# Optimization experiments

Measured on AMD Instinct MI355X. Metric: run time of the kernel, lower is better.

## Reference

```python
import jax, jax.numpy as jnp
import numpy as np

D = 1024
H = 16
HD = D // H


def setup_inputs() -> dict:
    key = jax.random.key(0)
    ks = jax.random.split(key, 9)
    s = 1.0 / np.sqrt(D)
    x = jax.random.normal(ks[0], (2, 2048, D), dtype=jnp.float32)
    Wq = jax.random.uniform(ks[1], (D, D), jnp.float32, -s, s)
    bq = jax.random.uniform(ks[2], (D,), jnp.float32, -s, s)
    Wk = jax.random.uniform(ks[3], (D, D), jnp.float32, -s, s)
    bk = jax.random.uniform(ks[4], (D,), jnp.float32, -s, s)
    Wv = jax.random.uniform(ks[5], (D, D), jnp.float32, -s, s)
    bv = jax.random.uniform(ks[6], (D,), jnp.float32, -s, s)
    Wo = jax.random.uniform(ks[7], (D, D), jnp.float32, -s, s)
    bo = jax.random.uniform(ks[8], (D,), jnp.float32, -s, s)
    return {"x": x, "Wq": Wq, "bq": bq, "Wk": Wk, "bk": bk,
            "Wv": Wv, "bv": bv, "Wo": Wo, "bo": bo}


def reference(x, Wq, bq, Wk, bk, Wv, bv, Wo, bo):
    B, S, _ = x.shape
    # project and split heads -> [B, H, S, HD]
    def split(t):
        return t.reshape(B, S, H, HD).transpose(0, 2, 1, 3)
    q = split(x @ Wq + bq)
    k = split(x @ Wk + bk)
    v = split(x @ Wv + bv)
    scores = jnp.einsum('bhqd,bhkd->bhqk', q, k) / np.sqrt(HD).astype(np.float32)
    attn = jax.nn.softmax(scores, axis=-1)
    ctx = jnp.einsum('bhqk,bhkd->bhqd', attn, v)  # [B,H,S,HD]
    ctx = ctx.transpose(0, 2, 1, 3).reshape(B, S, D)
    return ctx @ Wo + bo
```

## Files before the change

kernel.cpp:

```cpp
#include <hip/hip_runtime.h>
#include <hip/hip_bf16.h>
#include <math.h>

#define BB 2
#define SS 2048
#define DD 1024
#define HH 16
#define HD 64
#define MM (BB * SS)

typedef __bf16 bf16;
typedef __attribute__((ext_vector_type(8))) __bf16 bf16x8;
typedef __attribute__((ext_vector_type(4))) __bf16 bf16x4;
typedef __attribute__((ext_vector_type(4))) float f32x4;

#define QSCL 0.18033688011112042f

__device__ __forceinline__ void glds16(const bf16* g, bf16* l) {
    __builtin_amdgcn_global_load_lds(
        (const __attribute__((address_space(1))) void*)g,
        (__attribute__((address_space(3))) void*)l, 16, 0, 0);
}

__device__ __forceinline__ unsigned cvtpk_bf16(float a, float b) {
    unsigned r;
    asm("v_cvt_pk_bf16_f32 %0, %1, %2" : "=v"(r) : "v"(a), "v"(b));
    return r;
}

__global__ __launch_bounds__(256) void cvt_x(const float* __restrict__ x,
                                             bf16* __restrict__ xb) {
    int i = (blockIdx.x * 256 + threadIdx.x) * 4;
    float4 v = *(const float4*)(x + i);
    bf16x4 o;
    o[0] = (bf16)v.x; o[1] = (bf16)v.y; o[2] = (bf16)v.z; o[3] = (bf16)v.w;
    *(bf16x4*)(xb + i) = o;
}

__global__ __launch_bounds__(256) void cvt_w(
    const float* __restrict__ W0, const float* __restrict__ W1,
    const float* __restrict__ W2, const float* __restrict__ W3,
    bf16* __restrict__ Wt) {
    const float* W = (blockIdx.z == 0) ? W0 : (blockIdx.z == 1) ? W1
                   : (blockIdx.z == 2) ? W2 : W3;
    bf16* dst = Wt + (size_t)blockIdx.z * DD * DD;

    __shared__ float T[64][65];
    int k0 = blockIdx.y * 64, n0 = blockIdx.x * 64;
    int tr = threadIdx.x >> 4, tc = (threadIdx.x & 15) * 4;
#pragma unroll
    for (int u = 0; u < 4; u++) {
        int r = tr + u * 16;
        float4 v = *(const float4*)&W[(size_t)(k0 + r) * DD + n0 + tc];
        T[tc + 0][r] = v.x; T[tc + 1][r] = v.y;
        T[tc + 2][r] = v.z; T[tc + 3][r] = v.w;
    }
    __syncthreads();
#pragma unroll
    for (int u = 0; u < 4; u++) {
        int r = tr + u * 16;
        bf16x4 o;
        o[0] = (bf16)T[r][tc + 0]; o[1] = (bf16)T[r][tc + 1];
        o[2] = (bf16)T[r][tc + 2]; o[3] = (bf16)T[r][tc + 3];
        *(bf16x4*)&dst[(size_t)(n0 + r) * DD + k0 + tc] = o;
    }
}

__global__ __launch_bounds__(256) void vt_kernel(const bf16* __restrict__ V,
                                                 bf16* __restrict__ Vt) {
    const int bh = blockIdx.y;
    const int b = bh >> 4, h = bh & 15;
    const int s0 = blockIdx.x * 64;

    __shared__ bf16 T[64][72];
    const int r = threadIdx.x >> 2;
    const int c0 = (threadIdx.x & 3) * 16;

    const bf16* src = V + ((size_t)(b * SS + s0 + r)) * DD + h * HD + c0;
    *(bf16x8*)&T[r][c0]     = *(const bf16x8*)(src);
    *(bf16x8*)&T[r][c0 + 8] = *(const bf16x8*)(src + 8);
    __syncthreads();

    bf16x8 o0, o1;
#pragma unroll
    for (int i = 0; i < 8; i++) o0[i] = T[c0 + i][r];
#pragma unroll
    for (int i = 0; i < 8; i++) o1[i] = T[c0 + 8 + i][r];
    bf16* dst = Vt + ((size_t)bh * HD + r) * SS + s0 + c0;
    *(bf16x8*)dst       = o0;
    *(bf16x8*)(dst + 8) = o1;
}

__global__ __launch_bounds__(256) void mfma_gemm(
    const bf16* __restrict__ A, const bf16* __restrict__ Wt0,
    const float* __restrict__ b0, const float* __restrict__ b1,
    const float* __restrict__ b2,
    bf16* __restrict__ o0, bf16* __restrict__ o1, bf16* __restrict__ o2) {
    const int z = blockIdx.z;
    const bf16* Wt = Wt0 + (size_t)z * DD * DD;
    const float* bias = (z == 0) ? b0 : (z == 1) ? b1 : b2;
    bf16* dstb = (z == 0) ? o0 : (z == 1) ? o1 : o2;
    const float scl = (z == 0) ? QSCL : 1.0f;

    __shared__ __align__(16) bf16 As[128 * 64];
    __shared__ __align__(16) bf16 Bs[128 * 64];

    const int tid = threadIdx.x;
    const int lane = tid & 63;
    const int w = tid >> 6;
    const int l15 = lane & 15, quad = lane >> 4;
    const int m0 = blockIdx.y * 128;
    const int n0 = blockIdx.x * 128;
    const int mw = (w & 1) * 64;
    const int nw = (w >> 1) * 64;

    f32x4 acc[4][4];
#pragma unroll
    for (int i = 0; i < 4; i++)
#pragma unroll
        for (int j = 0; j < 4; j++) acc[i][j] = (f32x4){0.f, 0.f, 0.f, 0.f};

    for (int kt = 0; kt < DD; kt += 64) {
        __syncthreads();
#pragma unroll
        for (int u = 0; u < 4; u++) {
            int j = tid + u * 256;
            int row = j >> 3, cp = j & 7;
            int c = cp ^ (row & 7);
            glds16(A  + (size_t)(m0 + row) * DD + kt + c * 8, &As[j * 8]);
            glds16(Wt + (size_t)(n0 + row) * DD + kt + c * 8, &Bs[j * 8]);
        }
        __syncthreads();

#pragma unroll
        for (int kh = 0; kh < 2; kh++) {
            bf16x8 af[4], bf[4];
#pragma unroll
            for (int i = 0; i < 4; i++) {
                int ra = mw + i * 16 + l15;
                int ja = ra * 8 + ((kh * 4 + quad) ^ (ra & 7));
                af[i] = *(const bf16x8*)&As[ja * 8];
                int rb = nw + i * 16 + l15;
                int jb = rb * 8 + ((kh * 4 + quad) ^ (rb & 7));
                bf[i] = *(const bf16x8*)&Bs[jb * 8];
            }
#pragma unroll
            for (int i = 0; i < 4; i++)
#pragma unroll
                for (int j = 0; j < 4; j++)
                    acc[i][j] = __builtin_amdgcn_mfma_f32_16x16x32_bf16(
                        af[i], bf[j], acc[i][j], 0, 0, 0);
        }
    }

    float bcol[4];
#pragma unroll
    for (int j = 0; j < 4; j++) bcol[j] = bias[n0 + nw + j * 16 + l15];

#pragma unroll
    for (int i = 0; i < 4; i++)
#pragma unroll
        for (int j = 0; j < 4; j++)
#pragma unroll
            for (int r = 0; r < 4; r++) {
                int row = m0 + mw + i * 16 + quad * 4 + r;
                int col = n0 + nw + j * 16 + l15;
                dstb[(size_t)row * DD + col] =
                    (bf16)((acc[i][j][r] + bcol[j]) * scl);
            }
}

__global__ __launch_bounds__(256) void mfma_gemm_out(
    const bf16* __restrict__ A, const bf16* __restrict__ Wt,
    const float* __restrict__ bias, float* __restrict__ out) {
    __shared__ __align__(16) bf16 As[64 * 64];
    __shared__ __align__(16) bf16 Bs[128 * 64];

    const int tid = threadIdx.x;
    const int lane = tid & 63;
    const int w = tid >> 6;
    const int l15 = lane & 15, quad = lane >> 4;
    const int m0 = blockIdx.y * 64;
    const int n0 = blockIdx.x * 128;
    const int mw = (w & 1) * 32;
    const int nw = (w >> 1) * 64;

    f32x4 acc[2][4];
#pragma unroll
    for (int i = 0; i < 2; i++)
#pragma unroll
        for (int j = 0; j < 4; j++) acc[i][j] = (f32x4){0.f, 0.f, 0.f, 0.f};

    for (int kt = 0; kt < DD; kt += 64) {
        __syncthreads();
#pragma unroll
        for (int u = 0; u < 2; u++) {
            int j = tid + u * 256;
            int row = j >> 3, c = (j & 7) ^ (row & 7);
            glds16(A + (size_t)(m0 + row) * DD + kt + c * 8, &As[j * 8]);
        }
#pragma unroll
        for (int u = 0; u < 4; u++) {
            int j = tid + u * 256;
            int row = j >> 3, c = (j & 7) ^ (row & 7);
            glds16(Wt + (size_t)(n0 + row) * DD + kt + c * 8, &Bs[j * 8]);
        }
        __syncthreads();

#pragma unroll
        for (int kh = 0; kh < 2; kh++) {
            bf16x8 af[2], bf[4];
#pragma unroll
            for (int i = 0; i < 2; i++) {
                int ra = mw + i * 16 + l15;
                int ja = ra * 8 + ((kh * 4 + quad) ^ (ra & 7));
                af[i] = *(const bf16x8*)&As[ja * 8];
            }
#pragma unroll
            for (int j = 0; j < 4; j++) {
                int rb = nw + j * 16 + l15;
                int jb = rb * 8 + ((kh * 4 + quad) ^ (rb & 7));
                bf[j] = *(const bf16x8*)&Bs[jb * 8];
            }
#pragma unroll
            for (int i = 0; i < 2; i++)
#pragma unroll
                for (int j = 0; j < 4; j++)
                    acc[i][j] = __builtin_amdgcn_mfma_f32_16x16x32_bf16(
                        af[i], bf[j], acc[i][j], 0, 0, 0);
        }
    }

    float bcol[4];
#pragma unroll
    for (int j = 0; j < 4; j++) bcol[j] = bias[n0 + nw + j * 16 + l15];

#pragma unroll
    for (int i = 0; i < 2; i++)
#pragma unroll
        for (int j = 0; j < 4; j++)
#pragma unroll
            for (int r = 0; r < 4; r++) {
                int row = m0 + mw + i * 16 + quad * 4 + r;
                int col = n0 + nw + j * 16 + l15;
                out[(size_t)row * DD + col] = acc[i][j][r] + bcol[j];
            }
}

__global__ __launch_bounds__(256) void mfma_attn(
    const bf16* __restrict__ Qb, const bf16* __restrict__ Kb,
    const bf16* __restrict__ Vtg, bf16* __restrict__ ctxb) {
    __shared__ __align__(16) bf16 Ks[2][64 * 64];
    __shared__ __align__(16) bf16 Vs[2][64 * 64];
    __shared__ __align__(16) bf16 Ps[4][16 * 64];

    const int tid = threadIdx.x;
    const int lane = tid & 63;
    const int w = tid >> 6;
    const int l15 = lane & 15, quad = lane >> 4;
    const int bh = blockIdx.y;
    const int b = bh >> 4, h = bh & 15;
    const int q0 = blockIdx.x * 64;
    const size_t mb = (size_t)b * SS;
    const int hc = h * HD;
    const bf16* Vt_bh = Vtg + (size_t)bh * HD * SS;
    bf16* Pw = &Ps[w][0];

    bf16x8 qf[2];
#pragma unroll
    for (int kh = 0; kh < 2; kh++)
        qf[kh] = *(const bf16x8*)&Qb[(mb + q0 + w * 16 + l15) * DD +
                                     hc + kh * 32 + quad * 8];

    bf16x8 onev;
#pragma unroll
    for (int i = 0; i < 8; i++) onev[i] = (bf16)1.0f;

    int koff[4][2], voff[4][2], prd[2], pwr[4];
#pragma unroll
    for (int kb = 0; kb < 4; kb++) {
        int rk = kb * 16 + l15;
#pragma unroll
        for (int kh = 0; kh < 2; kh++)
            koff[kb][kh] = (rk * 8 + ((kh * 4 + quad) ^ (rk & 7))) * 8;
    }
#pragma unroll
    for (int nb = 0; nb < 4; nb++) {
        int rv = nb * 16 + l15;
#pragma unroll
        for (int kh = 0; kh < 2; kh++)
            voff[nb][kh] = (rv * 8 + ((kh * 4 + quad) ^ (rv & 7))) * 8;
    }
#pragma unroll
    for (int kh = 0; kh < 2; kh++)
        prd[kh] = l15 * 64 + (((kh * 4 + quad) ^ (l15 & 7)) << 3);
#pragma unroll
    for (int kb = 0; kb < 4; kb++) {
        int cw = kb * 2 + (quad >> 1);
        pwr[kb] = l15 * 64 + ((cw ^ (l15 & 7)) << 3) + (quad & 1) * 4;
    }

    const bf16* gK[2]; const bf16* gV[2]; int lo_[2];
#pragma unroll
    for (int u = 0; u < 2; u++) {
        int j = tid + u * 256;
        int row = j >> 3, cp = j & 7;
        int c = cp ^ (row & 7);
        gK[u] = Kb + (mb + row) * DD + hc + c * 8;
        gV[u] = Vt_bh + (size_t)row * SS + c * 8;
        lo_[u] = j * 8;
    }

    f32x4 o[4], lsum;
    lsum = (f32x4){0.f, 0.f, 0.f, 0.f};
#pragma unroll
    for (int nb = 0; nb < 4; nb++) o[nb] = (f32x4){0.f, 0.f, 0.f, 0.f};

#pragma unroll
    for (int u = 0; u < 2; u++) {
        glds16(gK[u], &Ks[0][lo_[u]]);  gK[u] += 64 * DD;
        glds16(gV[u], &Vs[0][lo_[u]]);  gV[u] += 64;
    }
    __syncthreads();

    for (int it = 0; it < SS / 64; ++it) {
        const int buf = it & 1;
        if (it + 1 < SS / 64) {
#pragma unroll
            for (int u = 0; u < 2; u++) {
                glds16(gK[u], &Ks[buf ^ 1][lo_[u]]);  gK[u] += 64 * DD;
                glds16(gV[u], &Vs[buf ^ 1][lo_[u]]);  gV[u] += 64;
            }
        }

        f32x4 sc[4];
#pragma unroll
        for (int kb = 0; kb < 4; kb++) sc[kb] = (f32x4){0.f, 0.f, 0.f, 0.f};
#pragma unroll
        for (int kb = 0; kb < 4; kb++)
#pragma unroll
            for (int kh = 0; kh < 2; kh++) {
                bf16x8 kf = *(const bf16x8*)&Ks[buf][koff[kb][kh]];
                sc[kb] = __builtin_amdgcn_mfma_f32_16x16x32_bf16(
                    kf, qf[kh], sc[kb], 0, 0, 0);
            }

#pragma unroll
        for (int kb = 0; kb < 4; kb++) {
            float p0 = exp2f(sc[kb][0]);
            float p1 = exp2f(sc[kb][1]);
            float p2 = exp2f(sc[kb][2]);
            float p3 = exp2f(sc[kb][3]);
            uint2 pu;
            pu.x = cvtpk_bf16(p0, p1);
            pu.y = cvtpk_bf16(p2, p3);
            *(uint2*)&Pw[pwr[kb]] = pu;
        }

#pragma unroll
        for (int kh = 0; kh < 2; kh++) {
            bf16x8 pf = *(const bf16x8*)&Pw[prd[kh]];
            lsum = __builtin_amdgcn_mfma_f32_16x16x32_bf16(
                pf, onev, lsum, 0, 0, 0);
#pragma unroll
            for (int nb = 0; nb < 4; nb++) {
                bf16x8 vf = *(const bf16x8*)&Vs[buf][voff[nb][kh]];
                o[nb] = __builtin_amdgcn_mfma_f32_16x16x32_bf16(
                    pf, vf, o[nb], 0, 0, 0);
            }
        }

        __syncthreads();
    }

    float li[4];
#pragma unroll
    for (int r = 0; r < 4; r++) li[r] = 1.0f / lsum[r];
#pragma unroll
    for (int nb = 0; nb < 4; nb++)
#pragma unroll
        for (int r = 0; r < 4; r++) {
            int qrow = q0 + w * 16 + quad * 4 + r;
            ctxb[(mb + qrow) * DD + hc + nb * 16 + l15] =
                (bf16)(o[nb][r] * li[r]);
        }
}

extern "C" void kernel_launch(void* const* d_in, const int* in_sizes, int n_in,
                              void* d_out, int out_size, void* d_ws, size_t ws_size,
                              hipStream_t stream) {
    const float* x  = (const float*)d_in[0];
    const float* Wq = (const float*)d_in[1];
    const float* bq = (const float*)d_in[2];
    const float* Wk = (const float*)d_in[3];
    const float* bk = (const float*)d_in[4];
    const float* Wv = (const float*)d_in[5];
    const float* bv = (const float*)d_in[6];
    const float* Wo = (const float*)d_in[7];
    const float* bo = (const float*)d_in[8];
    float* out = (float*)d_out;

    char* base = (char*)d_ws;
    bf16* xb   = (bf16*)(base);
    bf16* Wt   = (bf16*)(base + (8ull  << 20));
    bf16* Qb   = (bf16*)(base + (16ull << 20));
    bf16* Kb   = (bf16*)(base + (24ull << 20));
    bf16* Vb   = (bf16*)(base + (32ull << 20));
    bf16* ctxb = (bf16*)(base + (40ull << 20));
    bf16* Vtg  = xb;

    cvt_x<<<dim3((MM * DD) / (256 * 4)), dim3(256), 0, stream>>>(x, xb);
    cvt_w<<<dim3(16, 16, 4), dim3(256), 0, stream>>>(Wq, Wk, Wv, Wo, Wt);

    mfma_gemm<<<dim3(DD / 128, MM / 128, 3), dim3(256), 0, stream>>>(
        xb, Wt, bq, bk, bv, Qb, Kb, Vb);

    vt_kernel<<<dim3(SS / 64, BB * HH), dim3(256), 0, stream>>>(Vb, Vtg);

    mfma_attn<<<dim3(SS / 64, BB * HH), dim3(256), 0, stream>>>(Qb, Kb, Vtg, ctxb);

    mfma_gemm_out<<<dim3(DD / 128, MM / 64), dim3(256), 0, stream>>>(
        ctxb, Wt + 3ull * DD * DD, bo, out);
}
```

Baseline: 226.3 us.

## Keep softmax probabilities in registers by permuting V transpose layout

```diff
diff --git a/kernel.cpp b/kernel.cpp
--- a/kernel.cpp
+++ b/kernel.cpp
@@ -13,6 +13,7 @@
 typedef __attribute__((ext_vector_type(8))) __bf16 bf16x8;
 typedef __attribute__((ext_vector_type(4))) __bf16 bf16x4;
 typedef __attribute__((ext_vector_type(4))) float f32x4;
+typedef __attribute__((ext_vector_type(4))) unsigned u32x4;
 
 #define QSCL 0.18033688011112042f
 
@@ -74,18 +75,24 @@
 
     __shared__ bf16 T[64][72];
     const int r = threadIdx.x >> 2;
-    const int c0 = (threadIdx.x & 3) * 16;
+    const int C = threadIdx.x & 3;
+    const int c0 = C * 16;
 
     const bf16* src = V + ((size_t)(b * SS + s0 + r)) * DD + h * HD + c0;
     *(bf16x8*)&T[r][c0]     = *(const bf16x8*)(src);
     *(bf16x8*)&T[r][c0 + 8] = *(const bf16x8*)(src + 8);
     __syncthreads();
 
+    const int M0 = (C >> 1) * 32 + (C & 1) * 8;
     bf16x8 o0, o1;
 #pragma unroll
-    for (int i = 0; i < 8; i++) o0[i] = T[c0 + i][r];
-#pragma unroll
-    for (int i = 0; i < 8; i++) o1[i] = T[c0 + 8 + i][r];
+    for (int i = 0; i < 4; i++) o0[i]     = T[M0 + i][r];
+#pragma unroll
+    for (int i = 0; i < 4; i++) o0[4 + i] = T[M0 + 16 + i][r];
+#pragma unroll
+    for (int i = 0; i < 4; i++) o1[i]     = T[M0 + 4 + i][r];
+#pragma unroll
+    for (int i = 0; i < 4; i++) o1[4 + i] = T[M0 + 20 + i][r];
     bf16* dst = Vt + ((size_t)bh * HD + r) * SS + s0 + c0;
     *(bf16x8*)dst       = o0;
     *(bf16x8*)(dst + 8) = o1;
@@ -252,7 +259,6 @@
     const bf16* __restrict__ Vtg, bf16* __restrict__ ctxb) {
     __shared__ __align__(16) bf16 Ks[2][64 * 64];
     __shared__ __align__(16) bf16 Vs[2][64 * 64];
-    __shared__ __align__(16) bf16 Ps[4][16 * 64];
 
     const int tid = threadIdx.x;
     const int lane = tid & 63;
@@ -264,7 +270,6 @@
     const size_t mb = (size_t)b * SS;
     const int hc = h * HD;
     const bf16* Vt_bh = Vtg + (size_t)bh * HD * SS;
-    bf16* Pw = &Ps[w][0];
 
     bf16x8 qf[2];
 #pragma unroll
@@ -276,7 +281,7 @@
 #pragma unroll
     for (int i = 0; i < 8; i++) onev[i] = (bf16)1.0f;
 
-    int koff[4][2], voff[4][2], prd[2], pwr[4];
+    int koff[4][2], voff[4][2];
 #pragma unroll
     for (int kb = 0; kb < 4; kb++) {
         int rk = kb * 16 + l15;
@@ -290,14 +295,6 @@
 #pragma unroll
         for (int kh = 0; kh < 2; kh++)
             voff[nb][kh] = (rv * 8 + ((kh * 4 + quad) ^ (rv & 7))) * 8;
-    }
-#pragma unroll
-    for (int kh = 0; kh < 2; kh++)
-        prd[kh] = l15 * 64 + (((kh * 4 + quad) ^ (l15 & 7)) << 3);
-#pragma unroll
-    for (int kb = 0; kb < 4; kb++) {
-        int cw = kb * 2 + (quad >> 1);
-        pwr[kb] = l15 * 64 + ((cw ^ (l15 & 7)) << 3) + (quad & 1) * 4;
     }
 
     const bf16* gK[2]; const bf16* gV[2]; int lo_[2];
@@ -336,6 +333,7 @@
         f32x4 sc[4];
 #pragma unroll
         for (int kb = 0; kb < 4; kb++) sc[kb] = (f32x4){0.f, 0.f, 0.f, 0.f};
+        __builtin_amdgcn_s_setprio(1);
 #pragma unroll
         for (int kb = 0; kb < 4; kb++)
 #pragma unroll
@@ -344,31 +342,35 @@
                 sc[kb] = __builtin_amdgcn_mfma_f32_16x16x32_bf16(
                     kf, qf[kh], sc[kb], 0, 0, 0);
             }
-
+        __builtin_amdgcn_s_setprio(0);
+
+        u32x4 pw[2];
 #pragma unroll
         for (int kb = 0; kb < 4; kb++) {
             float p0 = exp2f(sc[kb][0]);
             float p1 = exp2f(sc[kb][1]);
             float p2 = exp2f(sc[kb][2]);
             float p3 = exp2f(sc[kb][3]);
-            uint2 pu;
-            pu.x = cvtpk_bf16(p0, p1);
-            pu.y = cvtpk_bf16(p2, p3);
-            *(uint2*)&Pw[pwr[kb]] = pu;
-        }
-
+            pw[kb >> 1][(kb & 1) * 2 + 0] = cvtpk_bf16(p0, p1);
+            pw[kb >> 1][(kb & 1) * 2 + 1] = cvtpk_bf16(p2, p3);
+        }
+        bf16x8 pfr[2];
+        pfr[0] = __builtin_bit_cast(bf16x8, pw[0]);
+        pfr[1] = __builtin_bit_cast(bf16x8, pw[1]);
+
+        __builtin_amdgcn_s_setprio(1);
 #pragma unroll
         for (int kh = 0; kh < 2; kh++) {
-            bf16x8 pf = *(const bf16x8*)&Pw[prd[kh]];
             lsum = __builtin_amdgcn_mfma_f32_16x16x32_bf16(
-                pf, onev, lsum, 0, 0, 0);
+                pfr[kh], onev, lsum, 0, 0, 0);
 #pragma unroll
             for (int nb = 0; nb < 4; nb++) {
                 bf16x8 vf = *(const bf16x8*)&Vs[buf][voff[nb][kh]];
                 o[nb] = __builtin_amdgcn_mfma_f32_16x16x32_bf16(
-                    pf, vf, o[nb], 0, 0, 0);
-            }
-        }
+                    pfr[kh], vf, o[nb], 0, 0, 0);
+            }
+        }
+        __builtin_amdgcn_s_setprio(0);
 
         __syncthreads();
     }
```

After: 222.8 us. No clear change (-1.5%).
